# Optimization experiments

Measured on AMD Instinct MI355X. Metric: run time of the kernel, lower is better.

Reference implementation:

```python
import jax, jax.numpy as jnp
import numpy as np

B, N, D, H = 8, 1025, 768, 12
PRE = 1            # prefix (CLS) tokens
P = N - PRE        # patch tokens
HD = D // H
EPS = 1e-6


def setup_inputs() -> dict:
    key = jax.random.key(0)
    ks = jax.random.split(key, 8)
    x = jax.random.normal(ks[0], (B, N, D), dtype=jnp.float32)
    graph = jax.random.uniform(ks[1], (B, P, P), dtype=jnp.float32)
    transferability = jax.random.uniform(ks[2], (B, P), dtype=jnp.float32)
    Wqkv = jax.random.normal(ks[3], (3 * D, D), dtype=jnp.float32) * 0.02
    bqkv = jnp.zeros((3 * D,), dtype=jnp.float32)
    Wproj = jax.random.normal(ks[4], (D, D), dtype=jnp.float32) * 0.02
    bproj = jnp.zeros((D,), dtype=jnp.float32)
    return {"x": x, "graph": graph, "transferability": transferability,
            "Wqkv": Wqkv, "bqkv": bqkv, "Wproj": Wproj, "bproj": bproj,
            "prefix_tokens": PRE}


def _build_mask(graph, transferability, prefix_tokens, n_tokens):
    # patch_weights: [B, P]
    pw = transferability / (jnp.sum(transferability, axis=1, keepdims=True) + EPS)
    b, p = pw.shape
    pre = prefix_tokens
    # Block layout: [[1s (pre,pre), pw broadcast (pre,P)], [pw[:,None] (P,pre), graph]]
    top_left = jnp.ones((b, pre, pre), dtype=graph.dtype)
    top_right = jnp.broadcast_to(pw[:, None, :], (b, pre, p))
    bot_left = jnp.broadcast_to(pw[:, :, None], (b, p, pre))
    top = jnp.concatenate([top_left, top_right], axis=2)
    bot = jnp.concatenate([bot_left, graph], axis=2)
    return jnp.concatenate([top, bot], axis=1)  # [B, N, N]


def reference(x, graph, transferability, Wqkv, bqkv, Wproj, bproj, prefix_tokens):
    bsz, n, d = x.shape
    scale = HD ** -0.5
    qkv = x @ Wqkv.T + bqkv                          # [B, N, 3D]
    qkv = qkv.reshape(bsz, n, 3, H, HD).transpose(2, 0, 3, 1, 4)  # [3, B, H, N, hd]
    q, k, v = qkv[0], qkv[1], qkv[2]
    attn = jax.nn.softmax(jnp.einsum('bhid,bhjd->bhij', q, k) * scale, axis=-1)
    mask = _build_mask(graph, transferability, prefix_tokens, n)  # [B, N, N]
    attn = attn * mask[:, None, :, :]
    attn = attn / (jnp.sum(attn, axis=-1, keepdims=True) + EPS)
    out = jnp.einsum('bhij,bhjd->bhid', attn, v)     # [B, H, N, hd]
    out = out.transpose(0, 2, 1, 3).reshape(bsz, n, d)
    return out @ Wproj.T + bproj
```

## Files before the change

kernel.cpp:

```cpp
#include <hip/hip_runtime.h>
#include <stdint.h>

constexpr int Bq = 8, Nn = 1025, Dd = 768, Hh = 12, HDd = 64, Pp = 1024;
constexpr int NP = 1088;
constexpr int MROWS = Bq * Nn;
constexpr float EPSI = 1e-6f;

typedef __attribute__((ext_vector_type(8))) short bfrag;
typedef __attribute__((ext_vector_type(4))) float ffrag;
typedef __attribute__((ext_vector_type(4))) float f4;
typedef __attribute__((ext_vector_type(4))) unsigned short us4;

#define MFMA16(a, b, c) __builtin_amdgcn_mfma_f32_16x16x32_bf16((a), (b), (c), 0, 0, 0)

#if __has_builtin(__builtin_amdgcn_exp2f)
#define EXP2(x) __builtin_amdgcn_exp2f(x)
#else
#define EXP2(x) exp2f(x)
#endif

__device__ __forceinline__ unsigned short f2bf(float f) {
  union { float f; uint32_t u; } v{f};
  uint32_t u = v.u;
  return (unsigned short)((u + 0x7fffu + ((u >> 16) & 1u)) >> 16);
}
__device__ __forceinline__ float bf2f(unsigned short s) {
  union { uint32_t u; float f; } v; v.u = ((uint32_t)s) << 16; return v.f;
}
__device__ __forceinline__ uint32_t pkbf(float a, float b) {
  uint32_t r;
  asm("v_cvt_pk_bf16_f32 %0, %1, %2" : "=v"(r) : "v"(a), "v"(b));
  return r;
}

__device__ __forceinline__ void gload16(const void* g, void* l) {
  __builtin_amdgcn_global_load_lds((const __attribute__((address_space(1))) unsigned int*)g,
                                   (__attribute__((address_space(3))) unsigned int*)l, 16, 0, 0);
}

__global__ __launch_bounds__(256) void conv_kernel(const float* __restrict__ src,
                                                   unsigned short* __restrict__ dst, int n4) {
  int idx = blockIdx.x * blockDim.x + threadIdx.x;
  int stride = gridDim.x * blockDim.x;
  for (int i = idx; i < n4; i += stride) {
    f4 v = ((const f4*)src)[i];
    us4 o; o[0] = f2bf(v[0]); o[1] = f2bf(v[1]); o[2] = f2bf(v[2]); o[3] = f2bf(v[3]);
    ((us4*)dst)[i] = o;
  }
}

__global__ __launch_bounds__(256) void pw_kernel(const float* __restrict__ tr, float* __restrict__ pw) {
  int b = blockIdx.x;
  __shared__ float red[256];
  float s = 0.f;
  for (int j = threadIdx.x; j < Pp; j += 256) s += tr[b * Pp + j];
  red[threadIdx.x] = s; __syncthreads();
  for (int o = 128; o > 0; o >>= 1) { if (threadIdx.x < o) red[threadIdx.x] += red[threadIdx.x + o]; __syncthreads(); }
  float inv = 1.f / (red[0] + EPSI);
  for (int j = threadIdx.x; j < Pp; j += 256) pw[b * Pp + j] = tr[b * Pp + j] * inv;
}

__global__ __launch_bounds__(256) void mask_kernel(const float* __restrict__ graph,
                                                   const float* __restrict__ pw,
                                                   unsigned short* __restrict__ mask) {
  int i = blockIdx.x, b = blockIdx.y;
  unsigned short* mrow = mask + ((size_t)b * NP + i) * NP;
  if (i >= Nn) { for (int j = threadIdx.x; j < NP; j += 256) mrow[j] = 0; return; }
  if (i == 0) {
    for (int j = threadIdx.x; j < NP; j += 256) {
      float v = (j == 0) ? 1.f : (j <= Pp ? pw[b * Pp + j - 1] : 0.f);
      mrow[j] = f2bf(v);
    }
  } else {
    const float* grow = graph + ((size_t)b * Pp + (i - 1)) * Pp;
    for (int j = threadIdx.x; j < NP; j += 256) {
      float v = (j == 0) ? pw[b * Pp + i - 1] : (j <= Pp ? grow[j - 1] : 0.f);
      mrow[j] = f2bf(v);
    }
  }
}

__global__ __launch_bounds__(256) void padzero_kernel(unsigned short* __restrict__ Qo,
                                                      unsigned short* __restrict__ Ko,
                                                      unsigned short* __restrict__ Vo) {
  int bh = blockIdx.x;
  unsigned short* qp = Qo + ((size_t)bh * NP + Nn) * 64;
  unsigned short* kp = Ko + ((size_t)bh * NP + Nn) * 64;
  for (int idx = threadIdx.x; idx < (NP - Nn) * 64; idx += 256) { qp[idx] = 0; kp[idx] = 0; }
  unsigned short* vp = Vo + (size_t)bh * 64 * NP;
  for (int idx = threadIdx.x; idx < 64 * (NP - Nn); idx += 256) {
    int d = idx / (NP - Nn), j = Nn + (idx - d * (NP - Nn));
    vp[(size_t)d * NP + j] = 0;
  }
}

__device__ __forceinline__ void gemm_main(const unsigned short* __restrict__ A, int rowA0, int rowAmax,
                                          const unsigned short* __restrict__ Bw, int rowB0,
                                          uint4* lds, ffrag acc[4][4], int tid) {
  const int l = tid & 63, lm = l & 15, lg = l >> 4, w = tid >> 6, wr = w >> 1, wc = w & 1;
  const unsigned short* aS[4]; const unsigned short* bS[4];
#pragma unroll
  for (int q = 0; q < 4; q++) {
    int c = tid + 256 * q, r = c >> 3, p = c & 7, g = p ^ (r & 7);
    int ra = rowA0 + r; if (ra > rowAmax) ra = rowAmax;
    aS[q] = A + (size_t)ra * 768 + 8 * g;
    bS[q] = Bw + (size_t)(rowB0 + r) * 768 + 8 * g;
  }
  uint4* ldsA = lds;
  uint4* ldsB = lds + 1024;
#pragma unroll 1
  for (int kt = 0; kt < 12; kt++) {
    __syncthreads();
#pragma unroll
    for (int q = 0; q < 4; q++) {
      gload16(aS[q], ldsA + tid + 256 * q); aS[q] += 64;
      gload16(bS[q], ldsB + tid + 256 * q); bS[q] += 64;
    }
    __syncthreads();
    const bfrag* LA = (const bfrag*)lds;
    const bfrag* LB = (const bfrag*)(lds + 1024);
    bfrag af[4][2], bf_[4][2];
#pragma unroll
    for (int am = 0; am < 4; am++) {
      int row = wr * 64 + am * 16 + lm;
      af[am][0] = LA[row * 8 + ((0 + lg) ^ (row & 7))];
      af[am][1] = LA[row * 8 + ((4 + lg) ^ (row & 7))];
    }
#pragma unroll
    for (int an = 0; an < 4; an++) {
      int row = wc * 64 + an * 16 + lm;
      bf_[an][0] = LB[row * 8 + ((0 + lg) ^ (row & 7))];
      bf_[an][1] = LB[row * 8 + ((4 + lg) ^ (row & 7))];
    }
#pragma unroll
    for (int am = 0; am < 4; am++)
#pragma unroll
      for (int an = 0; an < 4; an++) {
        acc[am][an] = MFMA16(af[am][0], bf_[an][0], acc[am][an]);
        acc[am][an] = MFMA16(af[am][1], bf_[an][1], acc[am][an]);
      }
  }
}

__global__ __launch_bounds__(256) void qkv_gemm_kernel(const unsigned short* __restrict__ X,
                                                       const unsigned short* __restrict__ W,
                                                       const float* __restrict__ bias,
                                                       unsigned short* __restrict__ Qo,
                                                       unsigned short* __restrict__ Ko,
                                                       unsigned short* __restrict__ Vo) {
  __shared__ uint4 lds[2048];
  int tid = threadIdx.x;
  ffrag zero4 = {0.f, 0.f, 0.f, 0.f};
  ffrag acc[4][4];
#pragma unroll
  for (int i = 0; i < 4; i++)
#pragma unroll
    for (int j = 0; j < 4; j++) acc[i][j] = zero4;
  gemm_main(X, blockIdx.x * 128, MROWS - 1, W, blockIdx.y * 128, lds, acc, tid);
  const int l = tid & 63, lm = l & 15, lg = l >> 4, w = tid >> 6, wr = w >> 1, wc = w & 1;
#pragma unroll
  for (int an = 0; an < 4; an++) {
    int gc = blockIdx.y * 128 + wc * 64 + an * 16 + lm;
    int which = gc / 768, rr = gc - which * 768, h = rr >> 6, hd = rr & 63;
    float bv = bias[gc];
#pragma unroll
    for (int am = 0; am < 4; am++) {
      int grb = blockIdx.x * 128 + wr * 64 + am * 16 + 4 * lg;
#pragma unroll
      for (int r = 0; r < 4; r++) {
        int gr = grb + r;
        if (gr >= MROWS) continue;
        int b = gr / Nn, i = gr - b * Nn;
        size_t bh = (size_t)(b * Hh + h);
        float v = acc[am][an][r] + bv;
        if (which == 0)      Qo[(bh * NP + i) * 64 + hd] = f2bf(v * 0.18033688f);
        else if (which == 1) Ko[(bh * NP + i) * 64 + hd] = f2bf(v);
        else                 Vo[(bh * 64 + hd) * NP + i] = f2bf(v);
      }
    }
  }
}

__global__ __launch_bounds__(256) void proj_gemm_kernel(const unsigned short* __restrict__ A,
                                                        const unsigned short* __restrict__ W,
                                                        const float* __restrict__ bias,
                                                        float* __restrict__ out) {
  __shared__ uint4 lds[2048];
  int tid = threadIdx.x;
  ffrag zero4 = {0.f, 0.f, 0.f, 0.f};
  ffrag acc[4][4];
#pragma unroll
  for (int i = 0; i < 4; i++)
#pragma unroll
    for (int j = 0; j < 4; j++) acc[i][j] = zero4;
  gemm_main(A, blockIdx.x * 128, MROWS - 1, W, blockIdx.y * 128, lds, acc, tid);
  const int l = tid & 63, lm = l & 15, lg = l >> 4, w = tid >> 6, wr = w >> 1, wc = w & 1;
#pragma unroll
  for (int an = 0; an < 4; an++) {
    int gc = blockIdx.y * 128 + wc * 64 + an * 16 + lm;
    float bv = bias[gc];
#pragma unroll
    for (int am = 0; am < 4; am++) {
      int grb = blockIdx.x * 128 + wr * 64 + am * 16 + 4 * lg;
#pragma unroll
      for (int r = 0; r < 4; r++) {
        int gr = grb + r;
        if (gr >= MROWS) continue;
        out[(size_t)gr * 768 + gc] = acc[am][an][r] + bv;
      }
    }
  }
}

__global__ __launch_bounds__(256) void attn_kernel(const unsigned short* __restrict__ Qg,
                                                   const unsigned short* __restrict__ Kg,
                                                   const unsigned short* __restrict__ Vg,
                                                   const unsigned short* __restrict__ Mg,
                                                   unsigned short* __restrict__ Og) {
  __shared__ uint4 smem[1536];
  int tid = threadIdx.x, w = tid >> 6, l = tid & 63, lm = l & 15, lg = l >> 4;
  int bx = blockIdx.x;
  int b = bx & 7, t5 = bx >> 3;
  int h = t5 % 12, ib = t5 / 12;
  size_t bh = (size_t)(b * Hh + h);
  const unsigned short* Qb = Qg + bh * NP * 64;
  const unsigned short* Kb = Kg + bh * NP * 64;
  const unsigned short* Vb = Vg + bh * 64 * NP;
  int i0 = ib * 64 + w * 16;
  int irow = i0 + lm;
  const unsigned short* Mrow = Mg + (size_t)b * NP * NP + (size_t)irow * NP;

  bfrag qf0 = *(const bfrag*)(Qb + (size_t)irow * 64 + 8 * lg);
  bfrag qf1 = *(const bfrag*)(Qb + (size_t)irow * 64 + 32 + 8 * lg);

  ffrag zero4 = {0.f, 0.f, 0.f, 0.f};
  ffrag oacc[4] = {zero4, zero4, zero4, zero4};
  float Zp = 0.f, Tp = 0.f;

  int rS = tid >> 3, pS = tid & 7, gS = pS ^ (rS & 7);
  const unsigned short* kS = Kb + rS * 64 + 8 * gS;
  const unsigned short* vS = Vb + (size_t)rS * NP + 8 * gS;
  uint4* ldsK4 = smem; uint4* ldsV4 = smem + 512;
  char* Pbase = (char*)(smem + 1024) + w * 2048;
  const bfrag* LK = (const bfrag*)ldsK4;
  const bfrag* LV = (const bfrag*)ldsV4;

#pragma unroll 1
  for (int t = 0; t < 17; t++) {
    uint4 k0 = *(const uint4*)kS, k1 = *(const uint4*)(kS + 2048);
    uint4 v0 = *(const uint4*)vS, v1 = *(const uint4*)(vS + 32 * NP);
    int j0 = t * 64;
    us4 mv[4];
#pragma unroll
    for (int jm = 0; jm < 4; jm++) mv[jm] = *(const us4*)(Mrow + j0 + 16 * jm + 4 * lg);
    __syncthreads();
    ldsK4[tid] = k0; ldsK4[tid + 256] = k1; ldsV4[tid] = v0; ldsV4[tid + 256] = v1;
    __syncthreads();
    kS += 64 * 64; vS += 64;

    ffrag s[4];
#pragma unroll
    for (int jm = 0; jm < 4; jm++) {
      int row = jm * 16 + lm;
      bfrag a0 = LK[row * 8 + ((0 + lg) ^ (row & 7))];
      bfrag a1 = LK[row * 8 + ((4 + lg) ^ (row & 7))];
      ffrag a = zero4;
      a = MFMA16(a0, qf0, a);
      a = MFMA16(a1, qf1, a);
      s[jm] = a;
    }
#pragma unroll
    for (int jm = 0; jm < 4; jm++) {
      float p0 = EXP2(s[jm][0]), p1 = EXP2(s[jm][1]), p2 = EXP2(s[jm][2]), p3 = EXP2(s[jm][3]);
      Zp += (p0 + p1) + (p2 + p3);
      float q0 = p0 * bf2f(mv[jm][0]), q1 = p1 * bf2f(mv[jm][1]);
      float q2 = p2 * bf2f(mv[jm][2]), q3 = p3 * bf2f(mv[jm][3]);
      Tp += (q0 + q1) + (q2 + q3);
      uint2 pk; pk.x = pkbf(q0, q1); pk.y = pkbf(q2, q3);
      int cpos = (((jm << 1) | (lg >> 1)) ^ (lm & 7));
      *(uint2*)(Pbase + lm * 128 + cpos * 16 + 8 * (lg & 1)) = pk;
    }
#pragma unroll
    for (int ks = 0; ks < 2; ks++) {
      bfrag pa = *(const bfrag*)(Pbase + lm * 128 + ((((ks << 2) | lg)) ^ (lm & 7)) * 16);
#pragma unroll
      for (int dm = 0; dm < 4; dm++) {
        int vrow = dm * 16 + lm;
        bfrag vb = LV[vrow * 8 + ((ks * 4 + lg) ^ (vrow & 7))];
        oacc[dm] = MFMA16(pa, vb, oacc[dm]);
      }
    }
  }
  Zp += __shfl_xor(Zp, 16); Zp += __shfl_xor(Zp, 32);
  Tp += __shfl_xor(Tp, 16); Tp += __shfl_xor(Tp, 32);
  float dn_row = 1.f / (Tp + EPSI * Zp);
  float dn[4];
#pragma unroll
  for (int r = 0; r < 4; r++) dn[r] = __shfl(dn_row, 4 * lg + r);
#pragma unroll
  for (int dm = 0; dm < 4; dm++)
#pragma unroll
    for (int r = 0; r < 4; r++) {
      int i = i0 + 4 * lg + r;
      if (i < Nn) Og[((size_t)(b * Nn + i)) * Dd + h * 64 + dm * 16 + lm] = f2bf(oacc[dm][r] * dn[r]);
    }
}

extern "C" void kernel_launch(void* const* d_in, const int* in_sizes, int n_in,
                              void* d_out, int out_size, void* d_ws, size_t ws_size,
                              hipStream_t stream) {
  const float* x      = (const float*)d_in[0];
  const float* graph  = (const float*)d_in[1];
  const float* transf = (const float*)d_in[2];
  const float* Wqkv   = (const float*)d_in[3];
  const float* bqkv   = (const float*)d_in[4];
  const float* Wproj  = (const float*)d_in[5];
  const float* bproj  = (const float*)d_in[6];
  float* out = (float*)d_out;
  char* ws = (char*)d_ws;

  unsigned short* xbf  = (unsigned short*)(ws + 0);
  unsigned short* wqb  = (unsigned short*)(ws + 12595200);
  unsigned short* wpb  = (unsigned short*)(ws + 16134144);
  unsigned short* Qb   = (unsigned short*)(ws + 17313792);
  unsigned short* Kb   = (unsigned short*)(ws + 30683136);
  unsigned short* Vb   = (unsigned short*)(ws + 44052480);
  float*          pw   = (float*)(ws + 57421824);
  unsigned short* mask = (unsigned short*)(ws + 57454592);
  unsigned short* aob  = xbf;

  conv_kernel<<<2048, 256, 0, stream>>>(x, xbf, (MROWS * Dd) / 4);
  conv_kernel<<<1728, 256, 0, stream>>>(Wqkv, wqb, (3 * Dd * Dd) / 4);
  conv_kernel<<<576, 256, 0, stream>>>(Wproj, wpb, (Dd * Dd) / 4);
  pw_kernel<<<Bq, 256, 0, stream>>>(transf, pw);
  mask_kernel<<<dim3(NP, Bq), 256, 0, stream>>>(graph, pw, mask);
  padzero_kernel<<<96, 256, 0, stream>>>(Qb, Kb, Vb);
  qkv_gemm_kernel<<<dim3(65, 18), 256, 0, stream>>>(xbf, wqb, bqkv, Qb, Kb, Vb);
  attn_kernel<<<1632, 256, 0, stream>>>(Qb, Kb, Vb, mask, aob);
  proj_gemm_kernel<<<dim3(65, 6), 256, 0, stream>>>(aob, wpb, bproj, out);
}
```

Before: 227.5 us.

## Double-buffer GEMM LDS tiles and remap workgroups for XCD locality

The shared GEMM main loop now keeps two LDS buffers and issues the direct-to-LDS global loads for the next K tile before running the MFMAs on the current one, with one wait and barrier per iteration instead of two syncs. Both GEMM kernels switch to a 1D grid and remap block IDs so each XCD gets a contiguous chunk of tiles, which should improve L2 reuse of the A and B panels. LDS use per block doubles to 64KB, which may lower occupancy, and the tile order is now row-major over the remapped index.

```diff
diff --git a/kernel.cpp b/kernel.cpp
--- a/kernel.cpp
+++ b/kernel.cpp
@@ -106,19 +106,31 @@
     aS[q] = A + (size_t)ra * 768 + 8 * g;
     bS[q] = Bw + (size_t)(rowB0 + r) * 768 + 8 * g;
   }
-  uint4* ldsA = lds;
-  uint4* ldsB = lds + 1024;
+  uint4* buf0 = lds;
+  uint4* buf1 = lds + 2048;
+#pragma unroll
+  for (int q = 0; q < 4; q++) {
+    gload16(aS[q], buf0 + tid + 256 * q);
+    gload16(bS[q], buf0 + 1024 + tid + 256 * q);
+    aS[q] += 64; bS[q] += 64;
+  }
+  asm volatile("s_waitcnt vmcnt(0)" ::: "memory");
+  __builtin_amdgcn_sched_barrier(0);
+  __builtin_amdgcn_s_barrier();
 #pragma unroll 1
   for (int kt = 0; kt < 12; kt++) {
-    __syncthreads();
-#pragma unroll
-    for (int q = 0; q < 4; q++) {
-      gload16(aS[q], ldsA + tid + 256 * q); aS[q] += 64;
-      gload16(bS[q], ldsB + tid + 256 * q); bS[q] += 64;
-    }
-    __syncthreads();
-    const bfrag* LA = (const bfrag*)lds;
-    const bfrag* LB = (const bfrag*)(lds + 1024);
+    uint4* cur = (kt & 1) ? buf1 : buf0;
+    uint4* nxt = (kt & 1) ? buf0 : buf1;
+    if (kt < 11) {
+#pragma unroll
+      for (int q = 0; q < 4; q++) {
+        gload16(aS[q], nxt + tid + 256 * q);
+        gload16(bS[q], nxt + 1024 + tid + 256 * q);
+        aS[q] += 64; bS[q] += 64;
+      }
+    }
+    const bfrag* LA = (const bfrag*)cur;
+    const bfrag* LB = (const bfrag*)(cur + 1024);
     bfrag af[4][2], bf_[4][2];
 #pragma unroll
     for (int am = 0; am < 4; am++) {
@@ -139,7 +151,17 @@
         acc[am][an] = MFMA16(af[am][0], bf_[an][0], acc[am][an]);
         acc[am][an] = MFMA16(af[am][1], bf_[an][1], acc[am][an]);
       }
-  }
+    asm volatile("s_waitcnt vmcnt(0)" ::: "memory");
+    __builtin_amdgcn_sched_barrier(0);
+    __builtin_amdgcn_s_barrier();
+  }
+}
+
+__device__ __forceinline__ int xcd_chunk_map(int orig, int nwg) {
+  int qq = nwg >> 3, rr = nwg & 7;
+  int xcd = orig & 7, idx = orig >> 3;
+  int base = (xcd < rr) ? xcd * (qq + 1) : rr * (qq + 1) + (xcd - rr) * qq;
+  return base + idx;
 }
 
 __global__ __launch_bounds__(256) void qkv_gemm_kernel(const unsigned short* __restrict__ X,
@@ -148,24 +170,26 @@
                                                        unsigned short* __restrict__ Qo,
                                                        unsigned short* __restrict__ Ko,
                                                        unsigned short* __restrict__ Vo) {
-  __shared__ uint4 lds[2048];
+  __shared__ uint4 lds[4096];
   int tid = threadIdx.x;
+  int wg = xcd_chunk_map(blockIdx.x, 65 * 18);
+  int xt = wg / 18, yt = wg - 18 * xt;
   ffrag zero4 = {0.f, 0.f, 0.f, 0.f};
   ffrag acc[4][4];
 #pragma unroll
   for (int i = 0; i < 4; i++)
 #pragma unroll
     for (int j = 0; j < 4; j++) acc[i][j] = zero4;
-  gemm_main(X, blockIdx.x * 128, MROWS - 1, W, blockIdx.y * 128, lds, acc, tid);
+  gemm_main(X, xt * 128, MROWS - 1, W, yt * 128, lds, acc, tid);
   const int l = tid & 63, lm = l & 15, lg = l >> 4, w = tid >> 6, wr = w >> 1, wc = w & 1;
 #pragma unroll
   for (int an = 0; an < 4; an++) {
-    int gc = blockIdx.y * 128 + wc * 64 + an * 16 + lm;
+    int gc = yt * 128 + wc * 64 + an * 16 + lm;
     int which = gc / 768, rr = gc - which * 768, h = rr >> 6, hd = rr & 63;
     float bv = bias[gc];
 #pragma unroll
     for (int am = 0; am < 4; am++) {
-      int grb = blockIdx.x * 128 + wr * 64 + am * 16 + 4 * lg;
+      int grb = xt * 128 + wr * 64 + am * 16 + 4 * lg;
 #pragma unroll
       for (int r = 0; r < 4; r++) {
         int gr = grb + r;
@@ -185,23 +209,25 @@
                                                         const unsigned short* __restrict__ W,
                                                         const float* __restrict__ bias,
                                                         float* __restrict__ out) {
-  __shared__ uint4 lds[2048];
+  __shared__ uint4 lds[4096];
   int tid = threadIdx.x;
+  int wg = xcd_chunk_map(blockIdx.x, 65 * 6);
+  int xt = wg / 6, yt = wg - 6 * xt;
   ffrag zero4 = {0.f, 0.f, 0.f, 0.f};
   ffrag acc[4][4];
 #pragma unroll
   for (int i = 0; i < 4; i++)
 #pragma unroll
     for (int j = 0; j < 4; j++) acc[i][j] = zero4;
-  gemm_main(A, blockIdx.x * 128, MROWS - 1, W, blockIdx.y * 128, lds, acc, tid);
+  gemm_main(A, xt * 128, MROWS - 1, W, yt * 128, lds, acc, tid);
   const int l = tid & 63, lm = l & 15, lg = l >> 4, w = tid >> 6, wr = w >> 1, wc = w & 1;
 #pragma unroll
   for (int an = 0; an < 4; an++) {
-    int gc = blockIdx.y * 128 + wc * 64 + an * 16 + lm;
+    int gc = yt * 128 + wc * 64 + an * 16 + lm;
     float bv = bias[gc];
 #pragma unroll
     for (int am = 0; am < 4; am++) {
-      int grb = blockIdx.x * 128 + wr * 64 + am * 16 + 4 * lg;
+      int grb = xt * 128 + wr * 64 + am * 16 + 4 * lg;
 #pragma unroll
       for (int r = 0; r < 4; r++) {
         int gr = grb + r;
@@ -335,7 +361,7 @@
   pw_kernel<<<Bq, 256, 0, stream>>>(transf, pw);
   mask_kernel<<<dim3(NP, Bq), 256, 0, stream>>>(graph, pw, mask);
   padzero_kernel<<<96, 256, 0, stream>>>(Qb, Kb, Vb);
-  qkv_gemm_kernel<<<dim3(65, 18), 256, 0, stream>>>(xbf, wqb, bqkv, Qb, Kb, Vb);
+  qkv_gemm_kernel<<<65 * 18, 256, 0, stream>>>(xbf, wqb, bqkv, Qb, Kb, Vb);
   attn_kernel<<<1632, 256, 0, stream>>>(Qb, Kb, Vb, mask, aob);
-  proj_gemm_kernel<<<dim3(65, 6), 256, 0, stream>>>(aob, wpb, bproj, out);
-}
+  proj_gemm_kernel<<<65 * 6, 256, 0, stream>>>(aob, wpb, bproj, out);
+}
```

Result: faster. 206.1 us (-9.4%).
